# Performance work log

Hardware: AMD Instinct MI355X
Metric: run time of the kernel (lower is better)

## Reference

```python
import jax, jax.numpy as jnp
import numpy as np
import math

B, C, K, H, W_SP = 16, 512, 64, 64, 64
STAGE_NUM = 2
THETA = 45


def _l2norm(x, axis):
    return x / (1e-6 + jnp.linalg.norm(x, axis=axis, keepdims=True))


def setup_inputs() -> dict:
    key = jax.random.key(0)
    k1, k2, k3, k4 = jax.random.split(key, 4)
    x = jax.random.normal(k1, (B, C, H, W_SP), dtype=jnp.float32)
    # conv1: 1x1 conv with bias, He init n = 1*1*C
    W1 = jax.random.normal(k2, (C, C), dtype=jnp.float32) * math.sqrt(2.0 / C)
    b1 = jnp.zeros((C,), dtype=jnp.float32)
    # conv2: 1x1 conv no bias + BN(gamma=1, beta=0)
    W2 = jax.random.normal(k3, (C, C), dtype=jnp.float32) * math.sqrt(2.0 / C)
    gamma = jnp.ones((C,), dtype=jnp.float32)
    beta = jnp.zeros((C,), dtype=jnp.float32)
    # mu buffer: normal(0, sqrt(2/k)), l2-normalized over channel dim
    mu0 = jax.random.normal(k4, (1, C, K), dtype=jnp.float32) * math.sqrt(2.0 / K)
    mu0 = _l2norm(mu0, axis=1)
    return {"x": x, "W1": W1, "b1": b1, "W2": W2, "gamma": gamma, "beta": beta, "mu0": mu0}


def reference(x, W1, b1, W2, gamma, beta, mu0):
    idn = x
    # conv1 (1x1)
    xc = jnp.einsum('bchw,oc->bohw', x, W1) + b1[None, :, None, None]
    b, c, h, w = xc.shape
    xf = xc.reshape(b, c, h * w)  # [b, c, n]
    mu = jnp.broadcast_to(mu0, (b, c, K))
    alpha0 = math.sin(math.radians(THETA)) ** 2
    beta0 = math.cos(math.radians(THETA)) ** 2
    v = K - 1
    # EM loop runs under torch.no_grad in the original -> stop_gradient
    xs = jax.lax.stop_gradient(xf)
    z = None
    for _ in range(STAGE_NUM):
        z = jnp.einsum('bcn,bck->bnk', xs, mu)  # [b, n, k]
        # V-E step: softmax / power-law blend
        z = alpha0 * jax.nn.softmax(z, axis=2) \
            + beta0 * (v + 1) / (v + 2.0 * jnp.linalg.norm(z, axis=2, keepdims=True))
        z_ = z / (1e-6 + z.sum(axis=1, keepdims=True))
        # V-M step
        mu = _l2norm(jnp.einsum('bcn,bnk->bck', xs, z_), axis=1)
    mu = jax.lax.stop_gradient(mu)
    z = jax.lax.stop_gradient(z)
    # reconstruction
    xr = jnp.einsum('bck,bnk->bcn', mu, z).reshape(b, c, h, w)
    xr = jax.nn.relu(xr)
    # conv2 (1x1, no bias) + BN (training-mode batch stats, eps=1e-5)
    y = jnp.einsum('bchw,oc->bohw', xr, W2)
    mean = y.mean(axis=(0, 2, 3))
    var = y.var(axis=(0, 2, 3))
    y = gamma[None, :, None, None] * (y - mean[None, :, None, None]) \
        * jax.lax.rsqrt(var + 1e-5)[None, :, None, None] + beta[None, :, None, None]
    out = jax.nn.relu(y + idn)
    return (out, mu, jnp.float32(THETA))
```

## Files before the change

kernel.cpp:

```cpp
#include <hip/hip_runtime.h>
#include <hip/hip_bf16.h>

#define B_ 16
#define C_ 512
#define K_ 64
#define N_ 4096
#define LDA 40

typedef unsigned short ushort_t;
typedef __attribute__((ext_vector_type(8))) short s16x8;
typedef __attribute__((ext_vector_type(4))) short s16x4;
typedef __attribute__((ext_vector_type(4))) float f32x4;

__device__ inline ushort_t f2bf(float f) {
    unsigned int u = __builtin_bit_cast(unsigned int, f);
    u = (u + 0x7FFFu + ((u >> 16) & 1u)) >> 16;
    return (ushort_t)u;
}
__device__ inline ushort_t f2bf_fast(float f) {
    unsigned int u = __builtin_bit_cast(unsigned int, f);
    return (ushort_t)((u + 0x8000u) >> 16);
}
__device__ inline float bf2f(ushort_t h) {
    unsigned int u = ((unsigned int)h) << 16;
    return __builtin_bit_cast(float, u);
}

template<int R>
__device__ inline void stage_tile(ushort_t* lds, const ushort_t* g, int gstride) {
    const int t = threadIdx.x;
    #pragma unroll
    for (int l = 0; l < R / 64; ++l) {
        int ch = t + l * 256;
        int row = ch >> 2, seg = ch & 3;
        s16x8 v = *(const s16x8*)(g + (size_t)row * gstride + seg * 8);
        *(s16x8*)(lds + row * LDA + seg * 8) = v;
    }
}

__device__ inline void stage_zf(ushort_t* lds, const float* g, int gstride) {
    const int t = threadIdx.x;
    #pragma unroll
    for (int l = 0; l < 2; ++l) {
        int ch = t + l * 256;
        int row = ch >> 3, seg = ch & 7;
        float4 f = *(const float4*)(g + (size_t)row * gstride + seg * 4);
        s16x4 v;
        v[0] = (short)f2bf(f.x); v[1] = (short)f2bf(f.y);
        v[2] = (short)f2bf(f.z); v[3] = (short)f2bf(f.w);
        *(s16x4*)(lds + row * LDA + seg * 4) = v;
    }
}

__global__ __launch_bounds__(256)
void cvtW_kernel(const float* __restrict__ W1, const float* __restrict__ W2,
                 ushort_t* __restrict__ W1b, ushort_t* __restrict__ W2b)
{
    int idx = blockIdx.x * 256 + threadIdx.x;
    const float* s; ushort_t* d; int off;
    if (idx < 32768) { s = W1; d = W1b; off = idx * 8; }
    else             { s = W2; d = W2b; off = (idx - 32768) * 8; }
    float4 a = *(const float4*)(s + off);
    float4 b = *(const float4*)(s + off + 4);
    s16x8 v;
    v[0] = (short)f2bf(a.x); v[1] = (short)f2bf(a.y);
    v[2] = (short)f2bf(a.z); v[3] = (short)f2bf(a.w);
    v[4] = (short)f2bf(b.x); v[5] = (short)f2bf(b.y);
    v[6] = (short)f2bf(b.z); v[7] = (short)f2bf(b.w);
    *(s16x8*)(d + off) = v;
}

__global__ __launch_bounds__(256)
void initmu_kernel(const float* __restrict__ mu0, ushort_t* __restrict__ mu_t)
{
    int idx = blockIdx.x * 256 + threadIdx.x;
    float v = mu0[idx];
    mu_t[(idx & 63) * C_ + (idx >> 6)] = f2bf(v);
}

__global__ __launch_bounds__(256)
void conv1_mfma(const ushort_t* __restrict__ W1b, const float* __restrict__ x,
                const float* __restrict__ b1, ushort_t* __restrict__ xf,
                ushort_t* __restrict__ xft)
{
    __shared__ ushort_t As[128 * LDA];
    __shared__ ushort_t Bs[128 * LDA];
    const int n0 = blockIdx.x * 128;
    const int o0 = blockIdx.y * 128;
    const int b  = blockIdx.z;
    const int t  = threadIdx.x;
    const int wid = t >> 6, lane = t & 63;
    const int wm = wid >> 1, wn = wid & 1;
    const int l15 = lane & 15, q = lane >> 4;

    const ushort_t* gA = W1b + (size_t)o0 * C_;
    const float*    xB = x + (size_t)b * C_ * N_ + n0;
    const int cg = t >> 5, ng = t & 31;

    f32x4 acc[4][4] = {};

    for (int c0 = 0; c0 < C_; c0 += 32) {
        __syncthreads();
        stage_tile<128>(As, gA + c0, C_);
        {
            const float* src = xB + (size_t)(c0 + cg * 4) * N_ + ng * 4;
            float4 f0 = *(const float4*)(src);
            float4 f1 = *(const float4*)(src + N_);
            float4 f2 = *(const float4*)(src + 2 * N_);
            float4 f3 = *(const float4*)(src + 3 * N_);
            ushort_t* dst = Bs + (ng * 4) * LDA + cg * 4;
            s16x4 v;
            v[0] = (short)f2bf_fast(f0.x); v[1] = (short)f2bf_fast(f1.x);
            v[2] = (short)f2bf_fast(f2.x); v[3] = (short)f2bf_fast(f3.x);
            *(s16x4*)(dst) = v;
            v[0] = (short)f2bf_fast(f0.y); v[1] = (short)f2bf_fast(f1.y);
            v[2] = (short)f2bf_fast(f2.y); v[3] = (short)f2bf_fast(f3.y);
            *(s16x4*)(dst + LDA) = v;
            v[0] = (short)f2bf_fast(f0.z); v[1] = (short)f2bf_fast(f1.z);
            v[2] = (short)f2bf_fast(f2.z); v[3] = (short)f2bf_fast(f3.z);
            *(s16x4*)(dst + 2 * LDA) = v;
            v[0] = (short)f2bf_fast(f0.w); v[1] = (short)f2bf_fast(f1.w);
            v[2] = (short)f2bf_fast(f2.w); v[3] = (short)f2bf_fast(f3.w);
            *(s16x4*)(dst + 3 * LDA) = v;
        }
        __syncthreads();
        s16x8 af[4], bf[4];
        #pragma unroll
        for (int m = 0; m < 4; ++m)
            af[m] = *(const s16x8*)&As[(wm * 64 + m * 16 + l15) * LDA + q * 8];
        #pragma unroll
        for (int n = 0; n < 4; ++n)
            bf[n] = *(const s16x8*)&Bs[(wn * 64 + n * 16 + l15) * LDA + q * 8];
        #pragma unroll
        for (int m = 0; m < 4; ++m)
            #pragma unroll
            for (int n = 0; n < 4; ++n)
                acc[m][n] = __builtin_amdgcn_mfma_f32_16x16x32_bf16(af[m], bf[n], acc[m][n], 0, 0, 0);
    }

    ushort_t* xfB  = xf  + (size_t)b * C_ * N_;
    ushort_t* xftB = xft + (size_t)b * N_ * C_;
    #pragma unroll
    for (int m = 0; m < 4; ++m) {
        int obase = o0 + wm * 64 + m * 16 + 4 * q;
        float bv[4];
        #pragma unroll
        for (int r = 0; r < 4; ++r) bv[r] = b1[obase + r];
        #pragma unroll
        for (int n = 0; n < 4; ++n) {
            int nn = n0 + wn * 64 + n * 16 + l15;
            s16x4 pk;
            #pragma unroll
            for (int r = 0; r < 4; ++r) {
                ushort_t h = f2bf(acc[m][n][r] + bv[r]);
                pk[r] = (short)h;
                xfB[(size_t)(obase + r) * N_ + nn] = h;
            }
            *(s16x4*)&xftB[(size_t)nn * C_ + obase] = pk;
        }
    }
}

__global__ __launch_bounds__(256)
void zgemm_mfma(const ushort_t* __restrict__ mu_t, const ushort_t* __restrict__ xft,
                float* __restrict__ zst, int mustride)
{
    __shared__ ushort_t As[64 * LDA];
    __shared__ ushort_t Bs[128 * LDA];
    const int n0 = blockIdx.x * 128;
    const int b  = blockIdx.z;
    const int t  = threadIdx.x;
    const int wid = t >> 6, lane = t & 63;
    const int wm = wid >> 1, wn = wid & 1;
    const int l15 = lane & 15, q = lane >> 4;

    const ushort_t* gA = mu_t + (size_t)b * mustride;
    const ushort_t* gB = xft + (size_t)b * N_ * C_ + (size_t)n0 * C_;

    f32x4 acc[2][4] = {};

    for (int c0 = 0; c0 < C_; c0 += 32) {
        __syncthreads();
        stage_tile<64>(As, gA + c0, C_);
        stage_tile<128>(Bs, gB + c0, C_);
        __syncthreads();
        s16x8 af[2], bf[4];
        #pragma unroll
        for (int m = 0; m < 2; ++m)
            af[m] = *(const s16x8*)&As[(wm * 32 + m * 16 + l15) * LDA + q * 8];
        #pragma unroll
        for (int n = 0; n < 4; ++n)
            bf[n] = *(const s16x8*)&Bs[(wn * 64 + n * 16 + l15) * LDA + q * 8];
        #pragma unroll
        for (int m = 0; m < 2; ++m)
            #pragma unroll
            for (int n = 0; n < 4; ++n)
                acc[m][n] = __builtin_amdgcn_mfma_f32_16x16x32_bf16(af[m], bf[n], acc[m][n], 0, 0, 0);
    }

    float* zB = zst + (size_t)b * K_ * N_;
    #pragma unroll
    for (int m = 0; m < 2; ++m) {
        int kbase = wm * 32 + m * 16 + 4 * q;
        #pragma unroll
        for (int n = 0; n < 4; ++n) {
            int nn = n0 + wn * 64 + n * 16 + l15;
            #pragma unroll
            for (int r = 0; r < 4; ++r)
                zB[(size_t)(kbase + r) * N_ + nn] = acc[m][n][r];
        }
    }
}

__global__ __launch_bounds__(256)
void softmax_col(float* __restrict__ zst)
{
    const int b = blockIdx.y;
    const int n = blockIdx.x * 256 + threadIdx.x;
    float* p = zst + (size_t)b * K_ * N_ + n;
    float v[K_];
    float m = -1e30f, sq = 0.f;
    #pragma unroll
    for (int k = 0; k < K_; ++k) {
        v[k] = p[(size_t)k * N_];
        m = fmaxf(m, v[k]);
        sq += v[k] * v[k];
    }
    float se = 0.f;
    #pragma unroll
    for (int k = 0; k < K_; ++k) { v[k] = expf(v[k] - m); se += v[k]; }
    float inv_se = 0.5f / se;
    float bl = 0.5f * (float)K_ / ((float)(K_ - 1) + 2.f * sqrtf(sq));
    #pragma unroll
    for (int k = 0; k < K_; ++k)
        p[(size_t)k * N_] = v[k] * inv_se + bl;
}

__global__ __launch_bounds__(256)
void colsum_t(const float* __restrict__ zst, float* __restrict__ invcs)
{
    int wid  = blockIdx.x * 4 + (threadIdx.x >> 6);
    int lane = threadIdx.x & 63;
    int b = wid >> 6, k = wid & 63;
    const float* p = zst + (size_t)b * K_ * N_ + (size_t)k * N_;
    float s = 0.f;
    #pragma unroll 8
    for (int i = 0; i < 64; ++i) s += p[lane + i * 64];
    #pragma unroll
    for (int off = 32; off > 0; off >>= 1) s += __shfl_xor(s, off);
    if (lane == 0) invcs[b * K_ + k] = 1.f / (1e-6f + s);
}

__global__ __launch_bounds__(256)
void mugemm_mfma(const float* __restrict__ zst, const ushort_t* __restrict__ xf,
                 const float* __restrict__ invcs, float* __restrict__ macc)
{
    __shared__ ushort_t As[64 * LDA];
    __shared__ ushort_t Bs[128 * LDA];
    const int ns = blockIdx.x * 512;
    const int c0 = blockIdx.y * 128;
    const int b  = blockIdx.z;
    const int t  = threadIdx.x;
    const int wid = t >> 6, lane = t & 63;
    const int wm = wid >> 1, wn = wid & 1;
    const int l15 = lane & 15, q = lane >> 4;

    const float*    gA = zst + (size_t)b * K_ * N_ + ns;
    const ushort_t* gB = xf + (size_t)b * C_ * N_ + (size_t)c0 * N_ + ns;

    f32x4 acc[2][4] = {};

    for (int nn0 = 0; nn0 < 512; nn0 += 32) {
        __syncthreads();
        stage_zf(As, gA + nn0, N_);
        stage_tile<128>(Bs, gB + nn0, N_);
        __syncthreads();
        s16x8 af[2], bf[4];
        #pragma unroll
        for (int m = 0; m < 2; ++m)
            af[m] = *(const s16x8*)&As[(wm * 32 + m * 16 + l15) * LDA + q * 8];
        #pragma unroll
        for (int n = 0; n < 4; ++n)
            bf[n] = *(const s16x8*)&Bs[(wn * 64 + n * 16 + l15) * LDA + q * 8];
        #pragma unroll
        for (int m = 0; m < 2; ++m)
            #pragma unroll
            for (int n = 0; n < 4; ++n)
                acc[m][n] = __builtin_amdgcn_mfma_f32_16x16x32_bf16(af[m], bf[n], acc[m][n], 0, 0, 0);
    }

    float* mB = macc + (size_t)b * K_ * C_;
    #pragma unroll
    for (int m = 0; m < 2; ++m) {
        int kbase = wm * 32 + m * 16 + 4 * q;
        float ic[4];
        #pragma unroll
        for (int r = 0; r < 4; ++r) ic[r] = invcs[b * K_ + kbase + r];
        #pragma unroll
        for (int n = 0; n < 4; ++n) {
            int cc = c0 + wn * 64 + n * 16 + l15;
            #pragma unroll
            for (int r = 0; r < 4; ++r)
                atomicAdd(&mB[(size_t)(kbase + r) * C_ + cc], acc[m][n][r] * ic[r]);
        }
    }
}

__global__ __launch_bounds__(256)
void l2norm_t(const float* __restrict__ macc, ushort_t* __restrict__ mu_t,
              ushort_t* __restrict__ mu_b, float* __restrict__ mu_out,
              float* __restrict__ theta_out)
{
    int wid  = blockIdx.x * 4 + (threadIdx.x >> 6);
    int lane = threadIdx.x & 63;
    int b = wid >> 6, k = wid & 63;
    const float* src = macc + (size_t)b * K_ * C_ + (size_t)k * C_;
    float v[8], s = 0.f;
    #pragma unroll
    for (int i = 0; i < 8; ++i) { v[i] = src[lane + i * 64]; s += v[i] * v[i]; }
    #pragma unroll
    for (int off = 32; off > 0; off >>= 1) s += __shfl_xor(s, off);
    float inv = 1.f / (1e-6f + sqrtf(s));
    ushort_t* mt = mu_t + (size_t)b * K_ * C_ + (size_t)k * C_;
    ushort_t* mb = mu_b + (size_t)b * C_ * K_ + k;
    float*    mo = mu_out + (size_t)b * C_ * K_ + k;
    #pragma unroll
    for (int i = 0; i < 8; ++i) {
        int c = lane + i * 64;
        float val = v[i] * inv;
        mt[c] = f2bf(val);
        mb[(size_t)c * K_] = f2bf(val);
        mo[(size_t)c * K_] = val;
    }
    if (wid == 0 && lane == 0) *theta_out = 45.0f;
}

__global__ __launch_bounds__(256)
void ztr_kernel(const float* __restrict__ zst, ushort_t* __restrict__ zs)
{
    __shared__ ushort_t lds[64 * 72];
    const int n0 = blockIdx.x * 64;
    const int b  = blockIdx.y;
    const int t  = threadIdx.x;
    const float* src = zst + (size_t)b * K_ * N_;
    #pragma unroll
    for (int i = 0; i < 4; ++i) {
        int ch = t + 256 * i;
        int krow = ch >> 4, seg = ch & 15;
        float4 f = *(const float4*)(src + (size_t)krow * N_ + n0 + seg * 4);
        lds[(seg * 4 + 0) * 72 + krow] = f2bf(f.x);
        lds[(seg * 4 + 1) * 72 + krow] = f2bf(f.y);
        lds[(seg * 4 + 2) * 72 + krow] = f2bf(f.z);
        lds[(seg * 4 + 3) * 72 + krow] = f2bf(f.w);
    }
    __syncthreads();
    ushort_t* dst = zs + (size_t)b * N_ * K_;
    #pragma unroll
    for (int i = 0; i < 2; ++i) {
        int ch = t + 256 * i;
        int row = ch >> 3, seg = ch & 7;
        s16x8 v = *(const s16x8*)&lds[row * 72 + seg * 8];
        *(s16x8*)(dst + (size_t)(n0 + row) * K_ + seg * 8) = v;
    }
}

__global__ __launch_bounds__(256)
void recon_mfma(const ushort_t* __restrict__ mu_b, const ushort_t* __restrict__ zs,
                ushort_t* __restrict__ xrt)
{
    __shared__ ushort_t As[128 * LDA];
    __shared__ ushort_t Bs[128 * LDA];
    const int n0 = blockIdx.x * 128;
    const int c0 = blockIdx.y * 128;
    const int b  = blockIdx.z;
    const int t  = threadIdx.x;
    const int wid = t >> 6, lane = t & 63;
    const int wm = wid >> 1, wn = wid & 1;
    const int l15 = lane & 15, q = lane >> 4;

    const ushort_t* gA = mu_b + (size_t)b * C_ * K_ + (size_t)c0 * K_;
    const ushort_t* gB = zs + (size_t)b * N_ * K_ + (size_t)n0 * K_;

    f32x4 acc[4][4] = {};

    for (int k0 = 0; k0 < K_; k0 += 32) {
        __syncthreads();
        stage_tile<128>(As, gA + k0, K_);
        stage_tile<128>(Bs, gB + k0, K_);
        __syncthreads();
        s16x8 af[4], bf[4];
        #pragma unroll
        for (int m = 0; m < 4; ++m)
            af[m] = *(const s16x8*)&As[(wm * 64 + m * 16 + l15) * LDA + q * 8];
        #pragma unroll
        for (int n = 0; n < 4; ++n)
            bf[n] = *(const s16x8*)&Bs[(wn * 64 + n * 16 + l15) * LDA + q * 8];
        #pragma unroll
        for (int m = 0; m < 4; ++m)
            #pragma unroll
            for (int n = 0; n < 4; ++n)
                acc[m][n] = __builtin_amdgcn_mfma_f32_16x16x32_bf16(af[m], bf[n], acc[m][n], 0, 0, 0);
    }

    ushort_t* xB = xrt + (size_t)b * N_ * C_;
    #pragma unroll
    for (int m = 0; m < 4; ++m) {
        int cbase = c0 + wm * 64 + m * 16 + 4 * q;
        #pragma unroll
        for (int n = 0; n < 4; ++n) {
            int nn = n0 + wn * 64 + n * 16 + l15;
            s16x4 pk;
            #pragma unroll
            for (int r = 0; r < 4; ++r)
                pk[r] = (short)f2bf(fmaxf(acc[m][n][r], 0.f));
            *(s16x4*)&xB[(size_t)nn * C_ + cbase] = pk;
        }
    }
}

__global__ __launch_bounds__(256)
void conv2_mfma(const ushort_t* __restrict__ W2b, const ushort_t* __restrict__ xrt,
                float* __restrict__ y)
{
    __shared__ ushort_t As[128 * LDA];
    __shared__ ushort_t Bs[128 * LDA];
    const int n0 = blockIdx.x * 128;
    const int o0 = blockIdx.y * 128;
    const int b  = blockIdx.z;
    const int t  = threadIdx.x;
    const int wid = t >> 6, lane = t & 63;
    const int wm = wid >> 1, wn = wid & 1;
    const int l15 = lane & 15, q = lane >> 4;

    const ushort_t* gA = W2b + (size_t)o0 * C_;
    const ushort_t* gB = xrt + (size_t)b * N_ * C_ + (size_t)n0 * C_;

    f32x4 acc[4][4] = {};

    for (int c0 = 0; c0 < C_; c0 += 32) {
        __syncthreads();
        stage_tile<128>(As, gA + c0, C_);
        stage_tile<128>(Bs, gB + c0, C_);
        __syncthreads();
        s16x8 af[4], bf[4];
        #pragma unroll
        for (int m = 0; m < 4; ++m)
            af[m] = *(const s16x8*)&As[(wm * 64 + m * 16 + l15) * LDA + q * 8];
        #pragma unroll
        for (int n = 0; n < 4; ++n)
            bf[n] = *(const s16x8*)&Bs[(wn * 64 + n * 16 + l15) * LDA + q * 8];
        #pragma unroll
        for (int m = 0; m < 4; ++m)
            #pragma unroll
            for (int n = 0; n < 4; ++n)
                acc[m][n] = __builtin_amdgcn_mfma_f32_16x16x32_bf16(af[m], bf[n], acc[m][n], 0, 0, 0);
    }

    float* yB = y + (size_t)b * C_ * N_;
    #pragma unroll
    for (int m = 0; m < 4; ++m) {
        int obase = o0 + wm * 64 + m * 16 + 4 * q;
        #pragma unroll
        for (int n = 0; n < 4; ++n) {
            int nn = n0 + wn * 64 + n * 16 + l15;
            #pragma unroll
            for (int r = 0; r < 4; ++r)
                yB[(size_t)(obase + r) * N_ + nn] = acc[m][n][r];
        }
    }
}

__global__ __launch_bounds__(256)
void bnstats_kernel(const float* __restrict__ y, const float* __restrict__ gamma,
                    const float* __restrict__ beta, float* __restrict__ bnscale,
                    float* __restrict__ bnshift)
{
    int o = blockIdx.x;
    int tid = threadIdx.x;
    float s = 0.f, sq = 0.f;
    for (int b = 0; b < B_; ++b) {
        const float4* p = (const float4*)(y + ((size_t)b * C_ + o) * N_);
        for (int i = tid; i < N_ / 4; i += 256) {
            float4 v = p[i];
            s  += v.x + v.y + v.z + v.w;
            sq += v.x * v.x + v.y * v.y + v.z * v.z + v.w * v.w;
        }
    }
    #pragma unroll
    for (int off = 32; off > 0; off >>= 1) {
        s  += __shfl_xor(s, off);
        sq += __shfl_xor(sq, off);
    }
    __shared__ float rs[4], rq[4];
    int wid = tid >> 6, lane = tid & 63;
    if (lane == 0) { rs[wid] = s; rq[wid] = sq; }
    __syncthreads();
    if (tid == 0) {
        float ts = rs[0] + rs[1] + rs[2] + rs[3];
        float tq = rq[0] + rq[1] + rq[2] + rq[3];
        const float inv_n = 1.f / (float)(B_ * N_);
        float mean = ts * inv_n;
        float var  = tq * inv_n - mean * mean;
        float istd = rsqrtf(var + 1e-5f);
        bnscale[o] = gamma[o] * istd;
        bnshift[o] = beta[o] - gamma[o] * istd * mean;
    }
}

__global__ __launch_bounds__(256)
void bnout_kernel(float* __restrict__ y, const float* __restrict__ x,
                  const float* __restrict__ bnscale, const float* __restrict__ bnshift)
{
    size_t i = (size_t)blockIdx.x * 256 + threadIdx.x;
    float4 vy = ((float4*)y)[i];
    float4 vx = ((const float4*)x)[i];
    int o = (int)((i >> 10) & (C_ - 1));
    float sc = bnscale[o], sh = bnshift[o];
    float4 r;
    r.x = fmaxf(fmaf(vy.x, sc, sh) + vx.x, 0.f);
    r.y = fmaxf(fmaf(vy.y, sc, sh) + vx.y, 0.f);
    r.z = fmaxf(fmaf(vy.z, sc, sh) + vx.z, 0.f);
    r.w = fmaxf(fmaf(vy.w, sc, sh) + vx.w, 0.f);
    ((float4*)y)[i] = r;
}

extern "C" void kernel_launch(void* const* d_in, const int* in_sizes, int n_in,
                              void* d_out, int out_size, void* d_ws, size_t ws_size,
                              hipStream_t stream)
{
    const float* x     = (const float*)d_in[0];
    const float* W1    = (const float*)d_in[1];
    const float* b1    = (const float*)d_in[2];
    const float* W2    = (const float*)d_in[3];
    const float* gamma = (const float*)d_in[4];
    const float* beta  = (const float*)d_in[5];
    const float* mu0   = (const float*)d_in[6];

    char* w = (char*)d_ws;
    ushort_t* xf   = (ushort_t*)w;  w += (size_t)B_ * C_ * N_ * 2;
    ushort_t* xft  = (ushort_t*)w;  w += (size_t)B_ * N_ * C_ * 2;
    ushort_t* zs   = (ushort_t*)w;  w += (size_t)B_ * N_ * K_ * 2;
    ushort_t* W1b  = (ushort_t*)w;  w += (size_t)C_ * C_ * 2;
    ushort_t* W2b  = (ushort_t*)w;  w += (size_t)C_ * C_ * 2;
    ushort_t* mu_t = (ushort_t*)w;  w += (size_t)B_ * K_ * C_ * 2;
    ushort_t* mu_b = (ushort_t*)w;  w += (size_t)B_ * C_ * K_ * 2;
    float* invcs   = (float*)w;     w += (size_t)B_ * K_ * 4;
    float* bnscale = (float*)w;     w += C_ * 4;
    float* bnshift = (float*)w;     w += C_ * 4;

    ushort_t* xrt = xf;

    float* y         = (float*)d_out;
    float* mu_out    = (float*)d_out + (size_t)B_ * C_ * N_;
    float* theta_out = mu_out + (size_t)B_ * C_ * K_;
    float* macc      = y;
    float* zst       = y + (size_t)8 * 1024 * 1024;

    cvtW_kernel<<<256, 256, 0, stream>>>(W1, W2, W1b, W2b);
    initmu_kernel<<<128, 256, 0, stream>>>(mu0, mu_t);

    conv1_mfma<<<dim3(32, 4, 16), 256, 0, stream>>>(W1b, x, b1, xf, xft);

    for (int s = 0; s < 2; ++s) {
        zgemm_mfma<<<dim3(32, 1, 16), 256, 0, stream>>>(mu_t, xft, zst, s == 0 ? 0 : K_ * C_);
        softmax_col<<<dim3(16, 16), 256, 0, stream>>>(zst);
        colsum_t<<<256, 256, 0, stream>>>(zst, invcs);
        hipMemsetAsync(macc, 0, (size_t)B_ * K_ * C_ * 4, stream);
        mugemm_mfma<<<dim3(8, 4, 16), 256, 0, stream>>>(zst, xf, invcs, macc);
        l2norm_t<<<256, 256, 0, stream>>>(macc, mu_t, mu_b, mu_out, theta_out);
    }

    ztr_kernel<<<dim3(64, 16), 256, 0, stream>>>(zst, zs);
    recon_mfma<<<dim3(32, 4, 16), 256, 0, stream>>>(mu_b, zs, xrt);
    conv2_mfma<<<dim3(32, 4, 16), 256, 0, stream>>>(W2b, xrt, y);
    bnstats_kernel<<<C_, 256, 0, stream>>>(y, gamma, beta, bnscale, bnshift);
    bnout_kernel<<<dim3(B_ * C_ * N_ / 4 / 256), 256, 0, stream>>>(y, x, bnscale, bnshift);
}
```

Measured before the change: 611.9 us.

## Fuse EM softmax/colsum/transpose into z-GEMM and BN stats into conv2 epilogue

The z-GEMM now finishes its tile in LDS, applies the softmax/power-law blend there, and writes bf16 z in both layouts while accumulating column sums with atomics. This replaces the separate softmax, colsum and transpose kernels and halves z traffic. Conv2 accumulates per-channel sum and sum-of-squares in its epilogue via atomics, so bnout derives scale and shift inline and the separate y-reading stats pass is dropped. The cost is lower z precision (bf16, fast exp), atomics, and a single-pass variance that can lose accuracy.

```diff
diff --git a/kernel.cpp b/kernel.cpp
--- a/kernel.cpp
+++ b/kernel.cpp
@@ -35,20 +35,6 @@
         int row = ch >> 2, seg = ch & 3;
         s16x8 v = *(const s16x8*)(g + (size_t)row * gstride + seg * 8);
         *(s16x8*)(lds + row * LDA + seg * 8) = v;
-    }
-}
-
-__device__ inline void stage_zf(ushort_t* lds, const float* g, int gstride) {
-    const int t = threadIdx.x;
-    #pragma unroll
-    for (int l = 0; l < 2; ++l) {
-        int ch = t + l * 256;
-        int row = ch >> 3, seg = ch & 7;
-        float4 f = *(const float4*)(g + (size_t)row * gstride + seg * 4);
-        s16x4 v;
-        v[0] = (short)f2bf(f.x); v[1] = (short)f2bf(f.y);
-        v[2] = (short)f2bf(f.z); v[3] = (short)f2bf(f.w);
-        *(s16x4*)(lds + row * LDA + seg * 4) = v;
     }
 }
 
@@ -162,13 +148,19 @@
 }
 
 __global__ __launch_bounds__(256)
-void zgemm_mfma(const ushort_t* __restrict__ mu_t, const ushort_t* __restrict__ xft,
-                float* __restrict__ zst, int mustride)
-{
-    __shared__ ushort_t As[64 * LDA];
-    __shared__ ushort_t Bs[128 * LDA];
+void zfused_mfma(const ushort_t* __restrict__ mu_t, const ushort_t* __restrict__ xft,
+                 ushort_t* __restrict__ zst, ushort_t* __restrict__ zs,
+                 float* __restrict__ cs, int mustride)
+{
+    __shared__ char pool[64 * 133 * 4 + 64 * 132 * 2 + 128 * 2 * 4];
+    float*    zt  = (float*)pool;
+    ushort_t* zb  = (ushort_t*)(pool + 64 * 133 * 4);
+    float*    csb = (float*)(pool + 64 * 133 * 4 + 64 * 132 * 2);
+    ushort_t* As  = (ushort_t*)pool;
+    ushort_t* Bs  = (ushort_t*)(pool + 64 * LDA * 2);
+
     const int n0 = blockIdx.x * 128;
-    const int b  = blockIdx.z;
+    const int b  = blockIdx.y;
     const int t  = threadIdx.x;
     const int wid = t >> 6, lane = t & 63;
     const int wm = wid >> 1, wn = wid & 1;
@@ -198,62 +190,79 @@
                 acc[m][n] = __builtin_amdgcn_mfma_f32_16x16x32_bf16(af[m], bf[n], acc[m][n], 0, 0, 0);
     }
 
-    float* zB = zst + (size_t)b * K_ * N_;
+    __syncthreads();
     #pragma unroll
     for (int m = 0; m < 2; ++m) {
         int kbase = wm * 32 + m * 16 + 4 * q;
         #pragma unroll
         for (int n = 0; n < 4; ++n) {
-            int nn = n0 + wn * 64 + n * 16 + l15;
+            int nl = wn * 64 + n * 16 + l15;
             #pragma unroll
             for (int r = 0; r < 4; ++r)
-                zB[(size_t)(kbase + r) * N_ + nn] = acc[m][n][r];
-        }
-    }
-}
-
-__global__ __launch_bounds__(256)
-void softmax_col(float* __restrict__ zst)
-{
-    const int b = blockIdx.y;
-    const int n = blockIdx.x * 256 + threadIdx.x;
-    float* p = zst + (size_t)b * K_ * N_ + n;
-    float v[K_];
-    float m = -1e30f, sq = 0.f;
-    #pragma unroll
-    for (int k = 0; k < K_; ++k) {
-        v[k] = p[(size_t)k * N_];
-        m = fmaxf(m, v[k]);
-        sq += v[k] * v[k];
-    }
-    float se = 0.f;
-    #pragma unroll
-    for (int k = 0; k < K_; ++k) { v[k] = expf(v[k] - m); se += v[k]; }
-    float inv_se = 0.5f / se;
-    float bl = 0.5f * (float)K_ / ((float)(K_ - 1) + 2.f * sqrtf(sq));
-    #pragma unroll
-    for (int k = 0; k < K_; ++k)
-        p[(size_t)k * N_] = v[k] * inv_se + bl;
-}
-
-__global__ __launch_bounds__(256)
-void colsum_t(const float* __restrict__ zst, float* __restrict__ invcs)
-{
-    int wid  = blockIdx.x * 4 + (threadIdx.x >> 6);
-    int lane = threadIdx.x & 63;
-    int b = wid >> 6, k = wid & 63;
-    const float* p = zst + (size_t)b * K_ * N_ + (size_t)k * N_;
-    float s = 0.f;
-    #pragma unroll 8
-    for (int i = 0; i < 64; ++i) s += p[lane + i * 64];
-    #pragma unroll
-    for (int off = 32; off > 0; off >>= 1) s += __shfl_xor(s, off);
-    if (lane == 0) invcs[b * K_ + k] = 1.f / (1e-6f + s);
-}
-
-__global__ __launch_bounds__(256)
-void mugemm_mfma(const float* __restrict__ zst, const ushort_t* __restrict__ xf,
-                 const float* __restrict__ invcs, float* __restrict__ macc)
+                zt[(kbase + r) * 133 + nl] = acc[m][n][r];
+        }
+    }
+    __syncthreads();
+    if (t < 128) {
+        const float* col = zt + t;
+        float mx = -1e30f, sq = 0.f;
+        #pragma unroll
+        for (int k = 0; k < K_; ++k) {
+            float v = col[k * 133];
+            mx = fmaxf(mx, v);
+            sq += v * v;
+        }
+        float se = 0.f;
+        #pragma unroll
+        for (int k = 0; k < K_; ++k) {
+            float e = __expf(col[k * 133] - mx);
+            se += e;
+            zb[k * 132 + t] = f2bf(e);
+        }
+        csb[t * 2]     = 0.5f / se;
+        csb[t * 2 + 1] = 0.5f * 64.f / (63.f + 2.f * sqrtf(sq));
+    }
+    __syncthreads();
+    ushort_t* zstB = zst + (size_t)b * K_ * N_;
+    #pragma unroll
+    for (int i = 0; i < 4; ++i) {
+        int ch = t + 256 * i;
+        int k = ch >> 4, seg = ch & 15;
+        s16x8 e8 = *(const s16x8*)&zb[k * 132 + seg * 8];
+        s16x8 o8;
+        float sum = 0.f;
+        #pragma unroll
+        for (int j = 0; j < 8; ++j) {
+            int nl = seg * 8 + j;
+            float v = fmaf(bf2f((ushort_t)e8[j]), csb[nl * 2], csb[nl * 2 + 1]);
+            sum += v;
+            o8[j] = (short)f2bf(v);
+        }
+        *(s16x8*)&zstB[(size_t)k * N_ + n0 + seg * 8] = o8;
+        #pragma unroll
+        for (int off = 1; off < 16; off <<= 1) sum += __shfl_xor(sum, off);
+        if ((t & 15) == 0) atomicAdd(&cs[b * K_ + k], sum);
+    }
+    ushort_t* zsB = zs + (size_t)b * N_ * K_;
+    #pragma unroll
+    for (int i = 0; i < 4; ++i) {
+        int ch = t + 256 * i;
+        int nl = ch >> 3, kseg = ch & 7;
+        float sc = csb[nl * 2], bl = csb[nl * 2 + 1];
+        s16x8 o8;
+        #pragma unroll
+        for (int j = 0; j < 8; ++j) {
+            int j2 = (j + nl) & 7;
+            float v = fmaf(bf2f(zb[(kseg * 8 + j2) * 132 + nl]), sc, bl);
+            o8[j2] = (short)f2bf(v);
+        }
+        *(s16x8*)&zsB[(size_t)(n0 + nl) * K_ + kseg * 8] = o8;
+    }
+}
+
+__global__ __launch_bounds__(256)
+void mugemm_mfma(const ushort_t* __restrict__ zst, const ushort_t* __restrict__ xf,
+                 const float* __restrict__ cs, float* __restrict__ macc)
 {
     __shared__ ushort_t As[64 * LDA];
     __shared__ ushort_t Bs[128 * LDA];
@@ -265,14 +274,14 @@
     const int wm = wid >> 1, wn = wid & 1;
     const int l15 = lane & 15, q = lane >> 4;
 
-    const float*    gA = zst + (size_t)b * K_ * N_ + ns;
+    const ushort_t* gA = zst + (size_t)b * K_ * N_ + ns;
     const ushort_t* gB = xf + (size_t)b * C_ * N_ + (size_t)c0 * N_ + ns;
 
     f32x4 acc[2][4] = {};
 
     for (int nn0 = 0; nn0 < 512; nn0 += 32) {
         __syncthreads();
-        stage_zf(As, gA + nn0, N_);
+        stage_tile<64>(As, gA + nn0, N_);
         stage_tile<128>(Bs, gB + nn0, N_);
         __syncthreads();
         s16x8 af[2], bf[4];
@@ -295,7 +304,7 @@
         int kbase = wm * 32 + m * 16 + 4 * q;
         float ic[4];
         #pragma unroll
-        for (int r = 0; r < 4; ++r) ic[r] = invcs[b * K_ + kbase + r];
+        for (int r = 0; r < 4; ++r) ic[r] = 1.f / (1e-6f + cs[b * K_ + kbase + r]);
         #pragma unroll
         for (int n = 0; n < 4; ++n) {
             int cc = c0 + wn * 64 + n * 16 + l15;
@@ -333,35 +342,6 @@
         mo[(size_t)c * K_] = val;
     }
     if (wid == 0 && lane == 0) *theta_out = 45.0f;
-}
-
-__global__ __launch_bounds__(256)
-void ztr_kernel(const float* __restrict__ zst, ushort_t* __restrict__ zs)
-{
-    __shared__ ushort_t lds[64 * 72];
-    const int n0 = blockIdx.x * 64;
-    const int b  = blockIdx.y;
-    const int t  = threadIdx.x;
-    const float* src = zst + (size_t)b * K_ * N_;
-    #pragma unroll
-    for (int i = 0; i < 4; ++i) {
-        int ch = t + 256 * i;
-        int krow = ch >> 4, seg = ch & 15;
-        float4 f = *(const float4*)(src + (size_t)krow * N_ + n0 + seg * 4);
-        lds[(seg * 4 + 0) * 72 + krow] = f2bf(f.x);
-        lds[(seg * 4 + 1) * 72 + krow] = f2bf(f.y);
-        lds[(seg * 4 + 2) * 72 + krow] = f2bf(f.z);
-        lds[(seg * 4 + 3) * 72 + krow] = f2bf(f.w);
-    }
-    __syncthreads();
-    ushort_t* dst = zs + (size_t)b * N_ * K_;
-    #pragma unroll
-    for (int i = 0; i < 2; ++i) {
-        int ch = t + 256 * i;
-        int row = ch >> 3, seg = ch & 7;
-        s16x8 v = *(const s16x8*)&lds[row * 72 + seg * 8];
-        *(s16x8*)(dst + (size_t)(n0 + row) * K_ + seg * 8) = v;
-    }
 }
 
 __global__ __launch_bounds__(256)
@@ -420,10 +400,11 @@
 
 __global__ __launch_bounds__(256)
 void conv2_mfma(const ushort_t* __restrict__ W2b, const ushort_t* __restrict__ xrt,
-                float* __restrict__ y)
+                float* __restrict__ y, float* __restrict__ ysum, float* __restrict__ ysq)
 {
     __shared__ ushort_t As[128 * LDA];
     __shared__ ushort_t Bs[128 * LDA];
+    __shared__ float sums[128][2];
     const int n0 = blockIdx.x * 128;
     const int o0 = blockIdx.y * 128;
     const int b  = blockIdx.z;
@@ -457,65 +438,77 @@
     }
 
     float* yB = y + (size_t)b * C_ * N_;
+    float ps[4][4], pq[4][4];
     #pragma unroll
     for (int m = 0; m < 4; ++m) {
         int obase = o0 + wm * 64 + m * 16 + 4 * q;
         #pragma unroll
+        for (int r = 0; r < 4; ++r) { ps[m][r] = 0.f; pq[m][r] = 0.f; }
+        #pragma unroll
         for (int n = 0; n < 4; ++n) {
             int nn = n0 + wn * 64 + n * 16 + l15;
             #pragma unroll
-            for (int r = 0; r < 4; ++r)
-                yB[(size_t)(obase + r) * N_ + nn] = acc[m][n][r];
-        }
-    }
-}
-
-__global__ __launch_bounds__(256)
-void bnstats_kernel(const float* __restrict__ y, const float* __restrict__ gamma,
-                    const float* __restrict__ beta, float* __restrict__ bnscale,
-                    float* __restrict__ bnshift)
-{
-    int o = blockIdx.x;
-    int tid = threadIdx.x;
-    float s = 0.f, sq = 0.f;
-    for (int b = 0; b < B_; ++b) {
-        const float4* p = (const float4*)(y + ((size_t)b * C_ + o) * N_);
-        for (int i = tid; i < N_ / 4; i += 256) {
-            float4 v = p[i];
-            s  += v.x + v.y + v.z + v.w;
-            sq += v.x * v.x + v.y * v.y + v.z * v.z + v.w * v.w;
-        }
-    }
-    #pragma unroll
-    for (int off = 32; off > 0; off >>= 1) {
-        s  += __shfl_xor(s, off);
-        sq += __shfl_xor(sq, off);
-    }
-    __shared__ float rs[4], rq[4];
-    int wid = tid >> 6, lane = tid & 63;
-    if (lane == 0) { rs[wid] = s; rq[wid] = sq; }
+            for (int r = 0; r < 4; ++r) {
+                float v = acc[m][n][r];
+                yB[(size_t)(obase + r) * N_ + nn] = v;
+                ps[m][r] += v;
+                pq[m][r] = fmaf(v, v, pq[m][r]);
+            }
+        }
+    }
+    #pragma unroll
+    for (int m = 0; m < 4; ++m)
+        #pragma unroll
+        for (int r = 0; r < 4; ++r)
+            #pragma unroll
+            for (int off = 1; off < 16; off <<= 1) {
+                ps[m][r] += __shfl_xor(ps[m][r], off);
+                pq[m][r] += __shfl_xor(pq[m][r], off);
+            }
     __syncthreads();
-    if (tid == 0) {
-        float ts = rs[0] + rs[1] + rs[2] + rs[3];
-        float tq = rq[0] + rq[1] + rq[2] + rq[3];
-        const float inv_n = 1.f / (float)(B_ * N_);
-        float mean = ts * inv_n;
-        float var  = tq * inv_n - mean * mean;
-        float istd = rsqrtf(var + 1e-5f);
-        bnscale[o] = gamma[o] * istd;
-        bnshift[o] = beta[o] - gamma[o] * istd * mean;
+    if (l15 == 0 && wn == 0) {
+        #pragma unroll
+        for (int m = 0; m < 4; ++m)
+            #pragma unroll
+            for (int r = 0; r < 4; ++r) {
+                int ol = wm * 64 + m * 16 + 4 * q + r;
+                sums[ol][0] = ps[m][r];
+                sums[ol][1] = pq[m][r];
+            }
+    }
+    __syncthreads();
+    if (l15 == 0 && wn == 1) {
+        #pragma unroll
+        for (int m = 0; m < 4; ++m)
+            #pragma unroll
+            for (int r = 0; r < 4; ++r) {
+                int ol = wm * 64 + m * 16 + 4 * q + r;
+                sums[ol][0] += ps[m][r];
+                sums[ol][1] += pq[m][r];
+            }
+    }
+    __syncthreads();
+    if (t < 128) {
+        atomicAdd(&ysum[o0 + t], sums[t][0]);
+        atomicAdd(&ysq[o0 + t],  sums[t][1]);
     }
 }
 
 __global__ __launch_bounds__(256)
 void bnout_kernel(float* __restrict__ y, const float* __restrict__ x,
-                  const float* __restrict__ bnscale, const float* __restrict__ bnshift)
+                  const float* __restrict__ gamma, const float* __restrict__ beta,
+                  const float* __restrict__ ysum, const float* __restrict__ ysq)
 {
     size_t i = (size_t)blockIdx.x * 256 + threadIdx.x;
     float4 vy = ((float4*)y)[i];
     float4 vx = ((const float4*)x)[i];
     int o = (int)((i >> 10) & (C_ - 1));
-    float sc = bnscale[o], sh = bnshift[o];
+    const float inv_n = 1.f / (float)(B_ * N_);
+    float mean = ysum[o] * inv_n;
+    float var  = ysq[o] * inv_n - mean * mean;
+    float istd = rsqrtf(var + 1e-5f);
+    float sc = gamma[o] * istd;
+    float sh = beta[o] - sc * mean;
     float4 r;
     r.x = fmaxf(fmaf(vy.x, sc, sh) + vx.x, 0.f);
     r.y = fmaxf(fmaf(vy.y, sc, sh) + vx.y, 0.f);
@@ -539,40 +532,38 @@
     char* w = (char*)d_ws;
     ushort_t* xf   = (ushort_t*)w;  w += (size_t)B_ * C_ * N_ * 2;
     ushort_t* xft  = (ushort_t*)w;  w += (size_t)B_ * N_ * C_ * 2;
-    ushort_t* zs   = (ushort_t*)w;  w += (size_t)B_ * N_ * K_ * 2;
     ushort_t* W1b  = (ushort_t*)w;  w += (size_t)C_ * C_ * 2;
     ushort_t* W2b  = (ushort_t*)w;  w += (size_t)C_ * C_ * 2;
     ushort_t* mu_t = (ushort_t*)w;  w += (size_t)B_ * K_ * C_ * 2;
     ushort_t* mu_b = (ushort_t*)w;  w += (size_t)B_ * C_ * K_ * 2;
-    float* invcs   = (float*)w;     w += (size_t)B_ * K_ * 4;
-    float* bnscale = (float*)w;     w += C_ * 4;
-    float* bnshift = (float*)w;     w += C_ * 4;
+    float* cs      = (float*)w;     w += (size_t)B_ * K_ * 4;
+    float* macc    = (float*)w;     w += (size_t)B_ * K_ * C_ * 4;
+    float* ysum    = (float*)w;     w += C_ * 4;
+    float* ysq     = (float*)w;     w += C_ * 4;
 
     ushort_t* xrt = xf;
 
     float* y         = (float*)d_out;
     float* mu_out    = (float*)d_out + (size_t)B_ * C_ * N_;
     float* theta_out = mu_out + (size_t)B_ * C_ * K_;
-    float* macc      = y;
-    float* zst       = y + (size_t)8 * 1024 * 1024;
+    ushort_t* zst = (ushort_t*)(y + (size_t)8  * 1024 * 1024);
+    ushort_t* zs  = (ushort_t*)(y + (size_t)16 * 1024 * 1024);
 
     cvtW_kernel<<<256, 256, 0, stream>>>(W1, W2, W1b, W2b);
     initmu_kernel<<<128, 256, 0, stream>>>(mu0, mu_t);
+    hipMemsetAsync(ysum, 0, 2 * C_ * 4, stream);
 
     conv1_mfma<<<dim3(32, 4, 16), 256, 0, stream>>>(W1b, x, b1, xf, xft);
 
     for (int s = 0; s < 2; ++s) {
-        zgemm_mfma<<<dim3(32, 1, 16), 256, 0, stream>>>(mu_t, xft, zst, s == 0 ? 0 : K_ * C_);
-        softmax_col<<<dim3(16, 16), 256, 0, stream>>>(zst);
-        colsum_t<<<256, 256, 0, stream>>>(zst, invcs);
-        hipMemsetAsync(macc, 0, (size_t)B_ * K_ * C_ * 4, stream);
-        mugemm_mfma<<<dim3(8, 4, 16), 256, 0, stream>>>(zst, xf, invcs, macc);
+        hipMemsetAsync(cs, 0, (size_t)B_ * K_ * 4 + (size_t)B_ * K_ * C_ * 4, stream);
+        zfused_mfma<<<dim3(32, 16), 256, 0, stream>>>(mu_t, xft, zst, zs, cs,
+                                                      s == 0 ? 0 : K_ * C_);
+        mugemm_mfma<<<dim3(8, 4, 16), 256, 0, stream>>>(zst, xf, cs, macc);
         l2norm_t<<<256, 256, 0, stream>>>(macc, mu_t, mu_b, mu_out, theta_out);
     }
 
-    ztr_kernel<<<dim3(64, 16), 256, 0, stream>>>(zst, zs);
     recon_mfma<<<dim3(32, 4, 16), 256, 0, stream>>>(mu_b, zs, xrt);
-    conv2_mfma<<<dim3(32, 4, 16), 256, 0, stream>>>(W2b, xrt, y);
-    bnstats_kernel<<<C_, 256, 0, stream>>>(y, gamma, beta, bnscale, bnshift);
-    bnout_kernel<<<dim3(B_ * C_ * N_ / 4 / 256), 256, 0, stream>>>(y, x, bnscale, bnshift);
-}
+    conv2_mfma<<<dim3(32, 4, 16), 256, 0, stream>>>(W2b, xrt, y, ysum, ysq);
+    bnout_kernel<<<dim3(B_ * C_ * N_ / 4 / 256), 256, 0, stream>>>(y, x, gamma, beta, ysum, ysq);
+}
```

New measurement: 573.4 us. 1.07x faster.
